# Kernel optimization log

Measured on AMD Instinct MI355X. Metric: run time of the kernel, lower is better.

Reference implementation:

```python
import jax, jax.numpy as jnp
import numpy as np

LEAKY_SLOPE = 0.2  # nn.LeakyReLU(alpha) with alpha=0.2
NEG_MASK = -9e15   # matches -9000000000000000.0 in the torch source


def _leaky_relu(x):
    return jnp.where(x > 0, x, LEAKY_SLOPE * x)


def setup_inputs() -> dict:
    key = jax.random.key(0)
    kh, ka, k0, k1, k2, k3 = jax.random.split(key, 6)
    B, N, D = 512, 256, 128
    hidden = jax.random.normal(kh, (B, N, D), dtype=jnp.float32)
    adj = jax.random.randint(ka, (B, N, N), 0, 5, dtype=jnp.int32)
    a_0 = jax.random.normal(k0, (D, 1), dtype=jnp.float32) * 0.05
    a_1 = jax.random.normal(k1, (D, 1), dtype=jnp.float32) * 0.05
    a_2 = jax.random.normal(k2, (D, 1), dtype=jnp.float32) * 0.05
    a_3 = jax.random.normal(k3, (D, 1), dtype=jnp.float32) * 0.05
    return {"hidden": hidden, "adj": adj, "a_0": a_0, "a_1": a_1, "a_2": a_2, "a_3": a_3}


def reference(hidden, adj, a_0, a_1, a_2, a_3):
    # hidden: [B, N, D]; adj: [B, N, N] int with relation ids in {0..4}
    # Original builds a_input[b,i,j,:] = hidden[b,i,:] * hidden[b,j,:] then
    # e_r = leakyrelu(a_input @ a_r). Equivalent (same math, no N*N*D blowup):
    # e_r[b,i,j] = leakyrelu( sum_d hidden[b,i,d] * a_r[d] * hidden[b,j,d] ).
    h = hidden

    def rel_scores(a_r):
        hw = h * a_r[:, 0][None, None, :]           # [B, N, D]
        return _leaky_relu(jnp.einsum('bid,bjd->bij', hw, h))  # [B, N, N]

    e_0 = rel_scores(a_0)
    e_1 = rel_scores(a_1)
    e_2 = rel_scores(a_2)
    e_3 = rel_scores(a_3)

    scores = jnp.full_like(e_0, NEG_MASK)
    scores = jnp.where(adj == 1, e_0, scores)
    scores = jnp.where(adj == 2, e_1, scores)
    scores = jnp.where(adj == 3, e_2, scores)
    scores = jnp.where(adj == 4, e_3, scores)

    alpha = jax.nn.softmax(scores, axis=-1)         # [B, N, N]
    return jnp.einsum('bij,bjd->bid', alpha, h)     # [B, N, D]
```

## Files before the change

kernel.cpp:

```cpp
#include <hip/hip_runtime.h>
#include <hip/hip_bf16.h>

typedef short bf16x8 __attribute__((ext_vector_type(8)));
typedef float f32x4  __attribute__((ext_vector_type(4)));
typedef __fp16 fp16x2 __attribute__((ext_vector_type(2)));

#define NB 512
#define NN 256
#define ND 128
#define H_STRIDE 136
#define HT_STRIDE 264
#define P_STRIDE 40
#define SMEM_SHORTS (NN*H_STRIDE + ND*HT_STRIDE + 8*2*16*P_STRIDE + 4*ND)
#define SMEM_BYTES (SMEM_SHORTS * 2)

__device__ __forceinline__ short f2b(float f) {
    union { float f; unsigned u; } v; v.f = f;
    unsigned r = v.u + 0x7fffu + ((v.u >> 16) & 1u);
    return (short)(r >> 16);
}
__device__ __forceinline__ float b2f(short s) {
    union { unsigned u; float f; } v; v.u = ((unsigned)(unsigned short)s) << 16;
    return v.f;
}
__device__ __forceinline__ unsigned pack_f16(float a, float b) {
    union { fp16x2 v; unsigned u; } x;
    x.v = __builtin_amdgcn_cvt_pkrtz(a, b);
    return x.u;
}
__device__ __forceinline__ float unp_lo(unsigned u) {
    union { unsigned short s; __fp16 h; } x; x.s = (unsigned short)(u & 0xffffu);
    return (float)x.h;
}
__device__ __forceinline__ float unp_hi(unsigned u) {
    union { unsigned short s; __fp16 h; } x; x.s = (unsigned short)(u >> 16);
    return (float)x.h;
}
__device__ __forceinline__ void lds_fence() {
    asm volatile("s_waitcnt lgkmcnt(0)" ::: "memory");
    __builtin_amdgcn_sched_barrier(0);
}

__global__ __attribute__((amdgpu_flat_work_group_size(512, 512)))
__attribute__((amdgpu_waves_per_eu(2, 2)))
void gat_fused(const float* __restrict__ hidden, const int* __restrict__ adj,
               const float* __restrict__ a0, const float* __restrict__ a1,
               const float* __restrict__ a2, const float* __restrict__ a3,
               float* __restrict__ out)
{
    extern __shared__ short smem[];
    short* s_h  = smem;
    short* s_ht = s_h + NN * H_STRIDE;
    short* s_p  = s_ht + ND * HT_STRIDE;
    short* s_a  = s_p + 8 * 2 * 16 * P_STRIDE;

    const int b    = blockIdx.x;
    const int tid  = threadIdx.x;
    const int wave = tid >> 6;
    const int lane = tid & 63;
    const int c = lane & 15;
    const int g = lane >> 4;

    const float* hb = hidden + (size_t)b * (NN * ND);
    for (int idx = tid * 4; idx < NN * ND; idx += 512 * 4) {
        const float4 v = *(const float4*)(hb + idx);
        const int j = idx >> 7, d = idx & (ND - 1);
        union { short s[4]; uint2 u; } pkv;
        pkv.s[0] = f2b(v.x); pkv.s[1] = f2b(v.y); pkv.s[2] = f2b(v.z); pkv.s[3] = f2b(v.w);
        *(uint2*)&s_h[j * H_STRIDE + d] = pkv.u;
    }
    {
        const float* ap = (tid < 128) ? a0 : (tid < 256) ? a1 : (tid < 384) ? a2 : a3;
        s_a[tid] = f2b(ap[tid & 127]);
    }
    __syncthreads();

    #pragma unroll
    for (int iter = 0; iter < 8; ++iter) {
        const int task = wave + 8 * iter;
        const int d0 = (task & 15) * 8;
        const int j0 = (task >> 4) * 64;
        union { short s[8]; uint4 u; } pkv;
        pkv.u = *(const uint4*)&s_h[(j0 + lane) * H_STRIDE + d0];
        #pragma unroll
        for (int e = 0; e < 8; ++e)
            s_ht[(d0 + e) * HT_STRIDE + j0 + lane] = pkv.s[e];
    }
    __syncthreads();

    short* s_pw = s_p + wave * (2 * 16 * P_STRIDE);
    const int* adj_b = adj + ((size_t)b << 16);
    float* out_b = out + (size_t)b * (NN * ND);

    for (int n = 0; n < 2; ++n) {
        const int it = wave + 8 * n;
        const int ibase = it * 16;

        unsigned avpk4[8];
        #pragma unroll
        for (int jt2 = 0; jt2 < 8; ++jt2) {
            const int4 aA = *(const int4*)&adj_b[(ibase + c) * NN + (2 * jt2) * 16 + 4 * g];
            const int4 aB = *(const int4*)&adj_b[(ibase + c) * NN + (2 * jt2 + 1) * 16 + 4 * g];
            avpk4[jt2] = (unsigned)aA.x | ((unsigned)aA.y << 4) |
                         ((unsigned)aA.z << 8) | ((unsigned)aA.w << 12) |
                         ((unsigned)aB.x << 16) | ((unsigned)aB.y << 20) |
                         ((unsigned)aB.z << 24) | ((unsigned)aB.w << 28);
        }
        __builtin_amdgcn_sched_barrier(0);

        unsigned scp[16][2];
        float m = -3.0e38f;

        {
            bf16x8 qs[2][4];
            #pragma unroll
            for (int s = 0; s < 4; ++s) {
                const bf16x8 q = *(const bf16x8*)&s_h[(ibase + c) * H_STRIDE + s * 32 + g * 8];
                #pragma unroll
                for (int r = 0; r < 2; ++r) {
                    const bf16x8 av = *(const bf16x8*)&s_a[r * ND + s * 32 + g * 8];
                    bf16x8 o;
                    #pragma unroll
                    for (int e = 0; e < 8; ++e) o[e] = f2b(b2f(q[e]) * b2f(av[e]));
                    qs[r][s] = o;
                }
            }
            #pragma unroll
            for (int jt = 0; jt < 16; ++jt) {
                if ((jt & 1) == 0) __builtin_amdgcn_sched_barrier(0);
                const int jbase = jt * 16;
                f32x4 e0 = {0.f,0.f,0.f,0.f}, e1 = {0.f,0.f,0.f,0.f};
                #pragma unroll
                for (int s = 0; s < 4; ++s) {
                    const bf16x8 hj = *(const bf16x8*)&s_h[(jbase + c) * H_STRIDE + s * 32 + g * 8];
                    e0 = __builtin_amdgcn_mfma_f32_16x16x32_bf16(hj, qs[0][s], e0, 0, 0, 0);
                    e1 = __builtin_amdgcn_mfma_f32_16x16x32_bf16(hj, qs[1][s], e1, 0, 0, 0);
                }
                const unsigned apk = avpk4[jt >> 1] >> ((jt & 1) * 16);
                float v[4];
                #pragma unroll
                for (int q = 0; q < 4; ++q) {
                    const int a = (apk >> (4 * q)) & 0xf;
                    v[q] = (a == 1) ? e0[q] : (a == 2) ? e1[q] : -9.0e15f;
                }
                scp[jt][0] = pack_f16(v[0], v[1]);
                scp[jt][1] = pack_f16(v[2], v[3]);
            }
        }

        {
            bf16x8 qs[2][4];
            #pragma unroll
            for (int s = 0; s < 4; ++s) {
                const bf16x8 q = *(const bf16x8*)&s_h[(ibase + c) * H_STRIDE + s * 32 + g * 8];
                #pragma unroll
                for (int r = 0; r < 2; ++r) {
                    const bf16x8 av = *(const bf16x8*)&s_a[(r + 2) * ND + s * 32 + g * 8];
                    bf16x8 o;
                    #pragma unroll
                    for (int e = 0; e < 8; ++e) o[e] = f2b(b2f(q[e]) * b2f(av[e]));
                    qs[r][s] = o;
                }
            }
            #pragma unroll
            for (int jt = 0; jt < 16; ++jt) {
                if ((jt & 1) == 0) __builtin_amdgcn_sched_barrier(0);
                const int jbase = jt * 16;
                f32x4 e2 = {0.f,0.f,0.f,0.f}, e3 = {0.f,0.f,0.f,0.f};
                #pragma unroll
                for (int s = 0; s < 4; ++s) {
                    const bf16x8 hj = *(const bf16x8*)&s_h[(jbase + c) * H_STRIDE + s * 32 + g * 8];
                    e2 = __builtin_amdgcn_mfma_f32_16x16x32_bf16(hj, qs[0][s], e2, 0, 0, 0);
                    e3 = __builtin_amdgcn_mfma_f32_16x16x32_bf16(hj, qs[1][s], e3, 0, 0, 0);
                }
                const unsigned apk = avpk4[jt >> 1] >> ((jt & 1) * 16);
                float v[4];
                #pragma unroll
                for (int q = 0; q < 4; ++q) {
                    const int a = (apk >> (4 * q)) & 0xf;
                    const float prev = (q == 0) ? unp_lo(scp[jt][0]) :
                                       (q == 1) ? unp_hi(scp[jt][0]) :
                                       (q == 2) ? unp_lo(scp[jt][1]) : unp_hi(scp[jt][1]);
                    float e = (a == 3) ? e2[q] : (a == 4) ? e3[q] : prev;
                    e = e > 0.f ? e : 0.2f * e;
                    m = fmaxf(m, e);
                    v[q] = e;
                }
                scp[jt][0] = pack_f16(v[0], v[1]);
                scp[jt][1] = pack_f16(v[2], v[3]);
            }
        }

        m = fmaxf(m, __shfl_xor(m, 16));
        m = fmaxf(m, __shfl_xor(m, 32));
        float sum = 0.f;
        #pragma unroll
        for (int jt = 0; jt < 16; ++jt) {
            const float p0 = __expf(unp_lo(scp[jt][0]) - m);
            const float p1 = __expf(unp_hi(scp[jt][0]) - m);
            const float p2 = __expf(unp_lo(scp[jt][1]) - m);
            const float p3 = __expf(unp_hi(scp[jt][1]) - m);
            sum += (p0 + p1) + (p2 + p3);
            scp[jt][0] = ((unsigned)(unsigned short)f2b(p0)) |
                         (((unsigned)(unsigned short)f2b(p1)) << 16);
            scp[jt][1] = ((unsigned)(unsigned short)f2b(p2)) |
                         (((unsigned)(unsigned short)f2b(p3)) << 16);
        }
        sum += __shfl_xor(sum, 16);
        sum += __shfl_xor(sum, 32);
        const float rinv = 1.f / sum;
        float rq[4];
        #pragma unroll
        for (int q = 0; q < 4; ++q) rq[q] = __shfl(rinv, 4 * g + q, 64);

        f32x4 oacc[8];
        #pragma unroll
        for (int dt = 0; dt < 8; ++dt) oacc[dt] = (f32x4){0.f,0.f,0.f,0.f};
        #pragma unroll
        for (int ph = 0; ph < 8; ++ph) {
            short* buf = s_pw + (ph & 1) * (16 * P_STRIDE);
            #pragma unroll
            for (int jj = 0; jj < 2; ++jj) {
                const int jt = 2 * ph + jj;
                uint2 w; w.x = scp[jt][0]; w.y = scp[jt][1];
                *(uint2*)&buf[c * P_STRIDE + jj * 16 + 4 * g] = w;
            }
            lds_fence();
            const bf16x8 pa = *(const bf16x8*)&buf[c * P_STRIDE + g * 8];
            #pragma unroll
            for (int dt = 0; dt < 8; ++dt) {
                const bf16x8 vb = *(const bf16x8*)
                    &s_ht[(dt * 16 + c) * HT_STRIDE + ph * 32 + g * 8];
                oacc[dt] = __builtin_amdgcn_mfma_f32_16x16x32_bf16(pa, vb, oacc[dt], 0, 0, 0);
            }
        }

        #pragma unroll
        for (int dt = 0; dt < 8; ++dt)
            #pragma unroll
            for (int q = 0; q < 4; ++q)
                out_b[(ibase + 4 * g + q) * ND + dt * 16 + c] = oacc[dt][q] * rq[q];
    }
}

extern "C" void kernel_launch(void* const* d_in, const int* in_sizes, int n_in,
                              void* d_out, int out_size, void* d_ws, size_t ws_size,
                              hipStream_t stream) {
    const float* hidden = (const float*)d_in[0];
    const int*   adjp   = (const int*)d_in[1];
    const float* a0 = (const float*)d_in[2];
    const float* a1 = (const float*)d_in[3];
    const float* a2 = (const float*)d_in[4];
    const float* a3 = (const float*)d_in[5];
    float* outp = (float*)d_out;

    (void)hipFuncSetAttribute((const void*)gat_fused,
                              hipFuncAttributeMaxDynamicSharedMemorySize, SMEM_BYTES);
    gat_fused<<<dim3(NB), dim3(512), SMEM_BYTES, stream>>>(hidden, adjp, a0, a1, a2, a3, outp);
}
```

Measured before the change: 90.91 us.

## Use 1024-thread blocks over two batches and shuffle P instead of LDS staging

Each block now has 1024 threads (16 waves), with one 16-row tile per wave, and loops over two batch items in sequence, so the grid is halved. The per-wave LDS staging buffer for the probability tile is replaced by cross-lane shuffles that build the MFMA A operand directly from registers. This removes the LDS round trip and its fence. In exchange, waves_per_eu rises to 4, which caps the register budget per wave and may cause spills, and the two batch items in a block are processed serially.

```diff
diff --git a/kernel.cpp b/kernel.cpp
--- a/kernel.cpp
+++ b/kernel.cpp
@@ -10,8 +10,7 @@
 #define ND 128
 #define H_STRIDE 136
 #define HT_STRIDE 264
-#define P_STRIDE 40
-#define SMEM_SHORTS (NN*H_STRIDE + ND*HT_STRIDE + 8*2*16*P_STRIDE + 4*ND)
+#define SMEM_SHORTS (NN*H_STRIDE + ND*HT_STRIDE + 4*ND)
 #define SMEM_BYTES (SMEM_SHORTS * 2)
 
 __device__ __forceinline__ short f2b(float f) {
@@ -36,13 +35,9 @@
     union { unsigned short s; __fp16 h; } x; x.s = (unsigned short)(u >> 16);
     return (float)x.h;
 }
-__device__ __forceinline__ void lds_fence() {
-    asm volatile("s_waitcnt lgkmcnt(0)" ::: "memory");
-    __builtin_amdgcn_sched_barrier(0);
-}
-
-__global__ __attribute__((amdgpu_flat_work_group_size(512, 512)))
-__attribute__((amdgpu_waves_per_eu(2, 2)))
+
+__global__ __attribute__((amdgpu_flat_work_group_size(1024, 1024)))
+__attribute__((amdgpu_waves_per_eu(4, 4)))
 void gat_fused(const float* __restrict__ hidden, const int* __restrict__ adj,
                const float* __restrict__ a0, const float* __restrict__ a1,
                const float* __restrict__ a2, const float* __restrict__ a3,
@@ -51,50 +46,52 @@
     extern __shared__ short smem[];
     short* s_h  = smem;
     short* s_ht = s_h + NN * H_STRIDE;
-    short* s_p  = s_ht + ND * HT_STRIDE;
-    short* s_a  = s_p + 8 * 2 * 16 * P_STRIDE;
-
-    const int b    = blockIdx.x;
+    short* s_a  = s_ht + ND * HT_STRIDE;
+
     const int tid  = threadIdx.x;
     const int wave = tid >> 6;
     const int lane = tid & 63;
     const int c = lane & 15;
     const int g = lane >> 4;
 
-    const float* hb = hidden + (size_t)b * (NN * ND);
-    for (int idx = tid * 4; idx < NN * ND; idx += 512 * 4) {
-        const float4 v = *(const float4*)(hb + idx);
-        const int j = idx >> 7, d = idx & (ND - 1);
-        union { short s[4]; uint2 u; } pkv;
-        pkv.s[0] = f2b(v.x); pkv.s[1] = f2b(v.y); pkv.s[2] = f2b(v.z); pkv.s[3] = f2b(v.w);
-        *(uint2*)&s_h[j * H_STRIDE + d] = pkv.u;
-    }
-    {
-        const float* ap = (tid < 128) ? a0 : (tid < 256) ? a1 : (tid < 384) ? a2 : a3;
-        s_a[tid] = f2b(ap[tid & 127]);
-    }
-    __syncthreads();
-
+    int srcl[4];
     #pragma unroll
-    for (int iter = 0; iter < 8; ++iter) {
-        const int task = wave + 8 * iter;
-        const int d0 = (task & 15) * 8;
-        const int j0 = (task >> 4) * 64;
-        union { short s[8]; uint4 u; } pkv;
-        pkv.u = *(const uint4*)&s_h[(j0 + lane) * H_STRIDE + d0];
-        #pragma unroll
-        for (int e = 0; e < 8; ++e)
-            s_ht[(d0 + e) * HT_STRIDE + j0 + lane] = pkv.s[e];
-    }
-    __syncthreads();
-
-    short* s_pw = s_p + wave * (2 * 16 * P_STRIDE);
-    const int* adj_b = adj + ((size_t)b << 16);
-    float* out_b = out + (size_t)b * (NN * ND);
-
-    for (int n = 0; n < 2; ++n) {
-        const int it = wave + 8 * n;
-        const int ibase = it * 16;
+    for (int r = 0; r < 4; ++r) srcl[r] = c + 16 * (((8 * g + 2 * r) & 15) >> 2);
+
+    for (int bb = 0; bb < 2; ++bb) {
+        const int b = (blockIdx.x << 1) | bb;
+        const float* hb = hidden + (size_t)b * (NN * ND);
+        if (bb) __syncthreads();
+
+        for (int idx = tid * 4; idx < NN * ND; idx += 1024 * 4) {
+            const float4 v = *(const float4*)(hb + idx);
+            const int j = idx >> 7, d = idx & (ND - 1);
+            union { short s[4]; uint2 u; } pkv;
+            pkv.s[0] = f2b(v.x); pkv.s[1] = f2b(v.y); pkv.s[2] = f2b(v.z); pkv.s[3] = f2b(v.w);
+            *(uint2*)&s_h[j * H_STRIDE + d] = pkv.u;
+        }
+        if (bb == 0 && tid < 512) {
+            const float* ap = (tid < 128) ? a0 : (tid < 256) ? a1 : (tid < 384) ? a2 : a3;
+            s_a[tid] = f2b(ap[tid & 127]);
+        }
+        __syncthreads();
+
+        #pragma unroll
+        for (int iter = 0; iter < 4; ++iter) {
+            const int task = wave + 16 * iter;
+            const int d0 = (task & 15) * 8;
+            const int j0 = (task >> 4) * 64;
+            union { short s[8]; uint4 u; } pkv;
+            pkv.u = *(const uint4*)&s_h[(j0 + lane) * H_STRIDE + d0];
+            #pragma unroll
+            for (int e = 0; e < 8; ++e)
+                s_ht[(d0 + e) * HT_STRIDE + j0 + lane] = pkv.s[e];
+        }
+        __syncthreads();
+
+        const int ibase = wave * 16;
+        const int* adj_b = adj + ((size_t)b << 16);
+        float* out_b = out + (size_t)b * (NN * ND);
 
         unsigned avpk4[8];
         #pragma unroll
@@ -218,20 +215,18 @@
         for (int dt = 0; dt < 8; ++dt) oacc[dt] = (f32x4){0.f,0.f,0.f,0.f};
         #pragma unroll
         for (int ph = 0; ph < 8; ++ph) {
-            short* buf = s_pw + (ph & 1) * (16 * P_STRIDE);
-            #pragma unroll
-            for (int jj = 0; jj < 2; ++jj) {
-                const int jt = 2 * ph + jj;
-                uint2 w; w.x = scp[jt][0]; w.y = scp[jt][1];
-                *(uint2*)&buf[c * P_STRIDE + jj * 16 + 4 * g] = w;
-            }
-            lds_fence();
-            const bf16x8 pa = *(const bf16x8*)&buf[c * P_STRIDE + g * 8];
+            union { unsigned u[4]; bf16x8 v; } pa;
+            #pragma unroll
+            for (int r = 0; r < 4; ++r) {
+                const unsigned lo = __shfl(scp[2 * ph][r & 1], srcl[r], 64);
+                const unsigned hi = __shfl(scp[2 * ph + 1][r & 1], srcl[r], 64);
+                pa.u[r] = (g >= 2) ? hi : lo;
+            }
             #pragma unroll
             for (int dt = 0; dt < 8; ++dt) {
                 const bf16x8 vb = *(const bf16x8*)
                     &s_ht[(dt * 16 + c) * HT_STRIDE + ph * 32 + g * 8];
-                oacc[dt] = __builtin_amdgcn_mfma_f32_16x16x32_bf16(pa, vb, oacc[dt], 0, 0, 0);
+                oacc[dt] = __builtin_amdgcn_mfma_f32_16x16x32_bf16(pa.v, vb, oacc[dt], 0, 0, 0);
             }
         }
 
@@ -256,5 +251,5 @@
 
     (void)hipFuncSetAttribute((const void*)gat_fused,
                               hipFuncAttributeMaxDynamicSharedMemorySize, SMEM_BYTES);
-    gat_fused<<<dim3(NB), dim3(512), SMEM_BYTES, stream>>>(hidden, adjp, a0, a1, a2, a3, outp);
-}
+    gat_fused<<<dim3(NB / 2), dim3(1024), SMEM_BYTES, stream>>>(hidden, adjp, a0, a1, a2, a3, outp);
+}
```

New measurement: 184.3 us. +102.8%, slower.
